# Kernel tuning notes

Measured on AMD Instinct MI355X. Metric: run time of the kernel, lower is better.

The kernel has to match this reference:

```python
import jax, jax.numpy as jnp
import numpy as np

DIM = 512
NUM_HEADS = 8
HEAD_DIM = DIM // NUM_HEADS
EPS = 1e-12  # F.normalize eps


def _l2norm(x):
    # F.normalize(x, dim=-1): x / max(||x||, eps)
    n = jnp.sqrt(jnp.sum(x * x, axis=-1, keepdims=True))
    return x / jnp.maximum(n, EPS)


def setup_inputs() -> dict:
    key = jax.random.key(0)
    ks = jax.random.split(key, 5)
    B, T, D = 4, 2048, DIM
    z = jax.random.normal(ks[0], (B, T, D), dtype=jnp.float32)
    t = jnp.zeros((1,), dtype=jnp.float32)  # unused ODE time
    omega = jax.random.normal(ks[1], (1, 1, D), dtype=jnp.float32) * 0.1
    # nn.Linear default init scale ~ U(-1/sqrt(fan_in), 1/sqrt(fan_in))
    s = 1.0 / np.sqrt(D)
    W_qk = jax.random.uniform(ks[2], (2 * D, D), jnp.float32, -s, s)
    W_out = jax.random.uniform(ks[3], (D, D), jnp.float32, -s, s)
    b_out = jax.random.uniform(ks[4], (D,), jnp.float32, -s, s)
    return {"t": t, "z": z, "omega": omega, "W_qk": W_qk, "W_out": W_out, "b_out": b_out}


def reference(t, z, omega, W_qk, W_out, b_out):
    B, T, D = z.shape
    H, hd = NUM_HEADS, HEAD_DIM
    qk = z @ W_qk.T                      # [B,T,2D]
    q, k = qk[..., :D], qk[..., D:]
    q = _l2norm(q.reshape(B, T, H, hd))  # [B,T,H,hd]
    k = _l2norm(k.reshape(B, T, H, hd))
    # coupling: [B,H,T,T]
    coupling = jnp.einsum("bqhd,bkhd->bhqk", q, k)
    interaction = jnp.sin(coupling)
    force = jnp.einsum("bhqk,bkhd->bqhd", interaction, k).reshape(B, T, D)
    return omega + force @ W_out.T + b_out
```

## Files before the change

kernel.cpp:

```cpp
#include <hip/hip_runtime.h>
#include <hip/hip_bf16.h>

typedef unsigned short u16;
typedef _Float16 f16;
typedef __attribute__((ext_vector_type(8))) _Float16 f16x8;
typedef __attribute__((ext_vector_type(2))) __fp16 h16x2;
typedef __attribute__((ext_vector_type(8))) short short8;
typedef __attribute__((ext_vector_type(4))) float f32x4;

#define B_ 4
#define T_ 2048
#define D_ 512
#define H_ 8
#define M_ (B_*T_)
#define INV2PI 0.15915494309189535f

__device__ f16 g_qb[M_*D_];
__device__ f16 g_kb[M_*D_];
__device__ f16 g_kTp[(size_t)B_*H_*64*T_];
__device__ f16 g_force[(size_t)M_*D_];

__device__ inline float sin2pi(float x) {
#if __has_builtin(__builtin_amdgcn_sinf)
  return __builtin_amdgcn_sinf(x);
#else
  return __sinf(x * 6.283185307179586f);
#endif
}

__device__ inline f16x8 cvt8h(f32x4 a, f32x4 b) {
  union { h16x2 h[4]; f16x8 v; } u;
  u.h[0] = __builtin_amdgcn_cvt_pkrtz(a[0], a[1]);
  u.h[1] = __builtin_amdgcn_cvt_pkrtz(a[2], a[3]);
  u.h[2] = __builtin_amdgcn_cvt_pkrtz(b[0], b[1]);
  u.h[3] = __builtin_amdgcn_cvt_pkrtz(b[2], b[3]);
  return u.v;
}

__device__ inline int perm5(int p) {
  int lg = p >> 3, e = p & 7;
  return (e < 4) ? lg*4 + e : 16 + lg*4 + (e & 3);
}

template<int MODE>
__global__ __launch_bounds__(256, 2)
void gemm_bt(float* __restrict__ Cout, const float* __restrict__ add1,
             const float* __restrict__ add2, const float* __restrict__ Afp,
             const float* __restrict__ Bfp) {
  constexpr int K = 512;
  constexpr int N = (MODE == 0) ? 1024 : 512;
  __shared__ f16 As[128*72];
  __shared__ f16 Bs[128*72];
  const int m0 = blockIdx.x*128, n0 = blockIdx.y*128;
  const int t = threadIdx.x;
  const int w = t>>6, l = t&63;
  const int wr = (w>>1)*64, wc = (w&1)*64;
  const int lg = l>>4, li = l&15;
  const int srow = t>>3, scol = (t&7)*8;

  f32x4 acc[4][4] = {};

  for (int k0 = 0; k0 < K; k0 += 64) {
#pragma unroll
    for (int p = 0; p < 4; ++p) {
      int r = srow + p*32;
      {
        f32x4 b0 = *(const f32x4*)&Bfp[(size_t)(n0+r)*K + k0 + scol];
        f32x4 b1 = *(const f32x4*)&Bfp[(size_t)(n0+r)*K + k0 + scol + 4];
        *(f16x8*)&Bs[r*72 + scol] = cvt8h(b0, b1);
      }
      if (MODE == 0) {
        f32x4 a0 = *(const f32x4*)&Afp[(size_t)(m0+r)*K + k0 + scol];
        f32x4 a1 = *(const f32x4*)&Afp[(size_t)(m0+r)*K + k0 + scol + 4];
        *(f16x8*)&As[r*72 + scol] = cvt8h(a0, a1);
      } else {
        *(short8*)&As[r*72 + scol] =
          *(const short8*)&g_force[(size_t)(m0+r)*K + k0 + scol];
      }
    }
    __syncthreads();
#pragma unroll
    for (int ks = 0; ks < 2; ++ks) {
      f16x8 af[4], bf[4];
#pragma unroll
      for (int i = 0; i < 4; ++i)
        af[i] = *(const f16x8*)&As[(wr + i*16 + li)*72 + ks*32 + lg*8];
#pragma unroll
      for (int j = 0; j < 4; ++j)
        bf[j] = *(const f16x8*)&Bs[(wc + j*16 + li)*72 + ks*32 + lg*8];
#pragma unroll
      for (int i = 0; i < 4; ++i)
#pragma unroll
        for (int j = 0; j < 4; ++j)
          acc[i][j] = __builtin_amdgcn_mfma_f32_16x16x32_f16(af[i], bf[j], acc[i][j], 0, 0, 0);
    }
    __syncthreads();
  }

  if (MODE == 0) {
    const bool isq = (n0 < 512);
    f16* dst = isq ? g_qb : g_kb;
    const float qs = isq ? INV2PI : 1.0f;
    const int nb = (isq ? n0 : n0 - 512) + wc;
#pragma unroll
    for (int i = 0; i < 4; ++i) {
#pragma unroll
      for (int r = 0; r < 4; ++r) {
        float s = 0.f;
#pragma unroll
        for (int j = 0; j < 4; ++j) s += acc[i][j][r]*acc[i][j][r];
#pragma unroll
        for (int off = 1; off < 16; off <<= 1) s += __shfl_xor(s, off);
        float sc = qs / fmaxf(sqrtf(s), 1e-12f);
        int row = m0 + wr + i*16 + lg*4 + r;
#pragma unroll
        for (int j = 0; j < 4; ++j)
          dst[(size_t)row*D_ + nb + j*16 + li] = (f16)(acc[i][j][r]*sc);
      }
    }
  } else {
#pragma unroll
    for (int i = 0; i < 4; ++i) {
#pragma unroll
      for (int j = 0; j < 4; ++j) {
        int col = n0 + wc + j*16 + li;
        float badd = add1[col] + add2[col];
#pragma unroll
        for (int r = 0; r < 4; ++r) {
          int row = m0 + wr + i*16 + lg*4 + r;
          Cout[(size_t)row*N + col] = acc[i][j][r] + badd;
        }
      }
    }
  }
}

__global__ void transpose_k_kernel() {
  __shared__ u16 tile[64*72];
  const int t0 = blockIdx.x*64, bh = blockIdx.y;
  const int b = bh>>3, h = bh&7;
  const int t = threadIdx.x;
  const u16* kb = (const u16*)g_kb;
  u16* kT = (u16*)g_kTp;
  {
    int r = t>>2, cs = (t&3)*16;
    const u16* src = kb + (size_t)(b*T_ + t0 + r)*D_ + h*64 + cs;
    *(short8*)&tile[r*72 + cs]     = *(const short8*)(src);
    *(short8*)&tile[r*72 + cs + 8] = *(const short8*)(src + 8);
  }
  __syncthreads();
  {
    int d = t>>2, ts = (t&3)*16;
    short8 o0, o1;
#pragma unroll
    for (int j = 0; j < 8; ++j) {
      int p0 = ts + j, p1 = ts + 8 + j;
      int s0 = (p0 & ~31) | perm5(p0 & 31);
      int s1 = (p1 & ~31) | perm5(p1 & 31);
      o0[j] = (short)tile[s0*72 + d];
      o1[j] = (short)tile[s1*72 + d];
    }
    u16* dst = kT + ((size_t)bh*64 + d)*T_ + t0 + ts;
    *(short8*)(dst)     = o0;
    *(short8*)(dst + 8) = o1;
  }
}

__global__ __launch_bounds__(256)
void kuramoto_attn_kernel() {
  __shared__ u16 Ks[2][128*72];
  __shared__ u16 KTs[2][64*136];
  const int wg  = blockIdx.x;
  const int wgp = (wg & 7)*32 + (wg >> 3);
  const int bh = wgp >> 3, qt = wgp & 7;
  const int b = bh >> 3, h = bh & 7;
  const int t = threadIdx.x;
  const int w = t>>6, l = t&63;
  const int lg = l>>4, li = l&15;

  f16x8 bq[2][4];
#pragma unroll
  for (int ks = 0; ks < 2; ++ks)
#pragma unroll
    for (int j = 0; j < 4; ++j)
      bq[ks][j] = *(const f16x8*)&g_qb[(size_t)(b*T_ + qt*256 + w*64 + j*16 + li)*D_
                                       + h*64 + ks*32 + lg*8];

  const int sr = t>>3, sc = (t&7)*8;
  const int sd = t>>4, sk = (t&15)*8;
  const u16* kbase = (const u16*)g_kb  + (size_t)b*T_*D_ + h*64;
  const u16* tbase = (const u16*)g_kTp + (size_t)bh*64*T_;

  f32x4 acc_o[4][4] = {};

#pragma unroll
  for (int p = 0; p < 4; ++p) {
    *(short8*)&Ks[0][(sr + p*32)*72 + sc] =
      *(const short8*)&kbase[(size_t)(sr + p*32)*D_ + sc];
    *(short8*)&KTs[0][(sd + p*16)*136 + sk] =
      *(const short8*)&tbase[(size_t)(sd + p*16)*T_ + sk];
  }
  __syncthreads();

#define QK_STEP(KKP, S) do {                                                   \
  _Pragma("unroll") for (int ks = 0; ks < 2; ++ks) {                           \
    f16x8 af0 = *(const f16x8*)&Ks[buf][((2*(KKP)  )*16 + li)*72 + ks*32 + lg*8]; \
    f16x8 af1 = *(const f16x8*)&Ks[buf][((2*(KKP)+1)*16 + li)*72 + ks*32 + lg*8]; \
    _Pragma("unroll") for (int j = 0; j < 4; ++j) {                            \
      S[0][j] = __builtin_amdgcn_mfma_f32_16x16x32_f16(af0, bq[ks][j], S[0][j], 0,0,0); \
      S[1][j] = __builtin_amdgcn_mfma_f32_16x16x32_f16(af1, bq[ks][j], S[1][j], 0,0,0); \
    } } } while(0)

#define SINPV_STEP(KKP, S) do {                                                \
  f16x8 apv[4];                                                                \
  _Pragma("unroll") for (int j = 0; j < 4; ++j) {                              \
    union { h16x2 h[4]; f16x8 v; } cv;                                         \
    cv.h[0] = __builtin_amdgcn_cvt_pkrtz(sin2pi(S[0][j][0]), sin2pi(S[0][j][1])); \
    cv.h[1] = __builtin_amdgcn_cvt_pkrtz(sin2pi(S[0][j][2]), sin2pi(S[0][j][3])); \
    cv.h[2] = __builtin_amdgcn_cvt_pkrtz(sin2pi(S[1][j][0]), sin2pi(S[1][j][1])); \
    cv.h[3] = __builtin_amdgcn_cvt_pkrtz(sin2pi(S[1][j][2]), sin2pi(S[1][j][3])); \
    apv[j] = cv.v; }                                                           \
  _Pragma("unroll") for (int di = 0; di < 4; ++di) {                           \
    f16x8 bv = *(const f16x8*)&KTs[buf][(di*16 + li)*136 + (KKP)*32 + lg*8];   \
    _Pragma("unroll") for (int j = 0; j < 4; ++j)                              \
      acc_o[j][di] = __builtin_amdgcn_mfma_f32_16x16x32_f16(apv[j], bv, acc_o[j][di], 0,0,0); \
  } } while(0)

#pragma unroll 2
  for (int ii = 0; ii < 16; ++ii) {
    const int buf = ii & 1;
    short8 rk[4], rt[4];
    if (ii < 15) {
      const int ktn = ii + 1;
#pragma unroll
      for (int p = 0; p < 4; ++p) {
        rk[p] = *(const short8*)&kbase[(size_t)(ktn*128 + sr + p*32)*D_ + sc];
        rt[p] = *(const short8*)&tbase[(size_t)(sd + p*16)*T_ + ktn*128 + sk];
      }
    }

    f32x4 sA[2][4] = {};
    f32x4 sB[2][4] = {};
    QK_STEP(0, sA);
    QK_STEP(1, sB);  SINPV_STEP(0, sA);
#pragma unroll
    for (int z = 0; z < 2; ++z)
#pragma unroll
      for (int j = 0; j < 4; ++j) sA[z][j] = (f32x4)(0.f);
    QK_STEP(2, sA);  SINPV_STEP(1, sB);
#pragma unroll
    for (int z = 0; z < 2; ++z)
#pragma unroll
      for (int j = 0; j < 4; ++j) sB[z][j] = (f32x4)(0.f);
    QK_STEP(3, sB);  SINPV_STEP(2, sA);
                     SINPV_STEP(3, sB);

    if (ii < 15) {
#pragma unroll
      for (int p = 0; p < 4; ++p) {
        *(short8*)&Ks[buf^1][(sr + p*32)*72 + sc] = rk[p];
        *(short8*)&KTs[buf^1][(sd + p*16)*136 + sk] = rt[p];
      }
    }
    __syncthreads();
  }
#undef QK_STEP
#undef SINPV_STEP

#pragma unroll
  for (int j = 0; j < 4; ++j)
#pragma unroll
    for (int di = 0; di < 4; ++di)
#pragma unroll
      for (int r = 0; r < 4; ++r) {
        int row = b*T_ + qt*256 + w*64 + j*16 + lg*4 + r;
        int col = h*64 + di*16 + li;
        g_force[(size_t)row*D_ + col] = (f16)acc_o[j][di][r];
      }
}

extern "C" void kernel_launch(void* const* d_in, const int* in_sizes, int n_in,
                              void* d_out, int out_size, void* d_ws, size_t ws_size,
                              hipStream_t stream) {
  const float* z     = (const float*)d_in[1];
  const float* omega = (const float*)d_in[2];
  const float* Wqk   = (const float*)d_in[3];
  const float* Wout  = (const float*)d_in[4];
  const float* bout  = (const float*)d_in[5];
  float* out = (float*)d_out;

  gemm_bt<0><<<dim3(M_/128, 1024/128), 256, 0, stream>>>(nullptr, nullptr, nullptr, z, Wqk);
  transpose_k_kernel<<<dim3(T_/64, B_*H_), 256, 0, stream>>>();
  kuramoto_attn_kernel<<<256, 256, 0, stream>>>();
  gemm_bt<1><<<dim3(M_/128, 512/128), 256, 0, stream>>>(out, omega, bout, nullptr, Wout);
}
```

Baseline: 155.3 us.

## Split attention over key halves and remap GEMM blocks across XCDs

The attention kernel now splits the key sequence into two halves, so 512 workgroups run instead of 256. Each half writes a partial force buffer, and the output GEMM adds the two when it loads its A operand. This is meant to fill the 256 CUs more evenly, which 256 workgroups did not. MFMA sections also get s_setprio hints, and the GEMM grids become 1D with an XCD-aware block mapping to improve L2 locality. The cost is an extra fp16 partial buffer, its write and read traffic, and fp16 rounding of two partial sums instead of one.

```diff
diff --git a/kernel.cpp b/kernel.cpp
--- a/kernel.cpp
+++ b/kernel.cpp
@@ -18,7 +18,8 @@
 __device__ f16 g_qb[M_*D_];
 __device__ f16 g_kb[M_*D_];
 __device__ f16 g_kTp[(size_t)B_*H_*64*T_];
-__device__ f16 g_force[(size_t)M_*D_];
+__device__ f16 g_fA[(size_t)M_*D_];
+__device__ f16 g_fB[(size_t)M_*D_];
 
 __device__ inline float sin2pi(float x) {
 #if __has_builtin(__builtin_amdgcn_sinf)
@@ -49,9 +50,14 @@
              const float* __restrict__ Bfp) {
   constexpr int K = 512;
   constexpr int N = (MODE == 0) ? 1024 : 512;
+  constexpr int NB = N/128;
   __shared__ f16 As[128*72];
   __shared__ f16 Bs[128*72];
-  const int m0 = blockIdx.x*128, n0 = blockIdx.y*128;
+  const int bidx = blockIdx.x;
+  const int xcd = bidx & 7, idx = bidx >> 3;
+  const int mp = xcd + 8*(idx/NB);
+  const int np = idx % NB;
+  const int m0 = mp*128, n0 = np*128;
   const int t = threadIdx.x;
   const int w = t>>6, l = t&63;
   const int wr = (w>>1)*64, wc = (w&1)*64;
@@ -74,8 +80,9 @@
         f32x4 a1 = *(const f32x4*)&Afp[(size_t)(m0+r)*K + k0 + scol + 4];
         *(f16x8*)&As[r*72 + scol] = cvt8h(a0, a1);
       } else {
-        *(short8*)&As[r*72 + scol] =
-          *(const short8*)&g_force[(size_t)(m0+r)*K + k0 + scol];
+        f16x8 a = *(const f16x8*)&g_fA[(size_t)(m0+r)*K + k0 + scol];
+        f16x8 c = *(const f16x8*)&g_fB[(size_t)(m0+r)*K + k0 + scol];
+        *(f16x8*)&As[r*72 + scol] = a + c;
       }
     }
     __syncthreads();
@@ -166,13 +173,13 @@
   }
 }
 
-__global__ __launch_bounds__(256)
+__global__ __launch_bounds__(256, 2)
 void kuramoto_attn_kernel() {
   __shared__ u16 Ks[2][128*72];
   __shared__ u16 KTs[2][64*136];
   const int wg  = blockIdx.x;
-  const int wgp = (wg & 7)*32 + (wg >> 3);
-  const int bh = wgp >> 3, qt = wgp & 7;
+  const int wgp = (wg & 7)*64 + (wg >> 3);
+  const int bh = wgp >> 4, qt = (wgp & 15) >> 1, kh = wgp & 1;
   const int b = bh >> 3, h = bh & 7;
   const int t = threadIdx.x;
   const int w = t>>6, l = t&63;
@@ -190,15 +197,16 @@
   const int sd = t>>4, sk = (t&15)*8;
   const u16* kbase = (const u16*)g_kb  + (size_t)b*T_*D_ + h*64;
   const u16* tbase = (const u16*)g_kTp + (size_t)bh*64*T_;
+  const int kt0 = kh*8;
 
   f32x4 acc_o[4][4] = {};
 
 #pragma unroll
   for (int p = 0; p < 4; ++p) {
     *(short8*)&Ks[0][(sr + p*32)*72 + sc] =
-      *(const short8*)&kbase[(size_t)(sr + p*32)*D_ + sc];
+      *(const short8*)&kbase[(size_t)(kt0*128 + sr + p*32)*D_ + sc];
     *(short8*)&KTs[0][(sd + p*16)*136 + sk] =
-      *(const short8*)&tbase[(size_t)(sd + p*16)*T_ + sk];
+      *(const short8*)&tbase[(size_t)(sd + p*16)*T_ + kt0*128 + sk];
   }
   __syncthreads();
 
@@ -206,10 +214,12 @@
   _Pragma("unroll") for (int ks = 0; ks < 2; ++ks) {                           \
     f16x8 af0 = *(const f16x8*)&Ks[buf][((2*(KKP)  )*16 + li)*72 + ks*32 + lg*8]; \
     f16x8 af1 = *(const f16x8*)&Ks[buf][((2*(KKP)+1)*16 + li)*72 + ks*32 + lg*8]; \
+    __builtin_amdgcn_s_setprio(1);                                             \
     _Pragma("unroll") for (int j = 0; j < 4; ++j) {                            \
       S[0][j] = __builtin_amdgcn_mfma_f32_16x16x32_f16(af0, bq[ks][j], S[0][j], 0,0,0); \
       S[1][j] = __builtin_amdgcn_mfma_f32_16x16x32_f16(af1, bq[ks][j], S[1][j], 0,0,0); \
-    } } } while(0)
+    }                                                                          \
+    __builtin_amdgcn_s_setprio(0); } } while(0)
 
 #define SINPV_STEP(KKP, S) do {                                                \
   f16x8 apv[4];                                                                \
@@ -222,16 +232,18 @@
     apv[j] = cv.v; }                                                           \
   _Pragma("unroll") for (int di = 0; di < 4; ++di) {                           \
     f16x8 bv = *(const f16x8*)&KTs[buf][(di*16 + li)*136 + (KKP)*32 + lg*8];   \
+    __builtin_amdgcn_s_setprio(1);                                             \
     _Pragma("unroll") for (int j = 0; j < 4; ++j)                              \
       acc_o[j][di] = __builtin_amdgcn_mfma_f32_16x16x32_f16(apv[j], bv, acc_o[j][di], 0,0,0); \
+    __builtin_amdgcn_s_setprio(0);                                             \
   } } while(0)
 
 #pragma unroll 2
-  for (int ii = 0; ii < 16; ++ii) {
+  for (int ii = 0; ii < 8; ++ii) {
     const int buf = ii & 1;
     short8 rk[4], rt[4];
-    if (ii < 15) {
-      const int ktn = ii + 1;
+    if (ii < 7) {
+      const int ktn = kt0 + ii + 1;
 #pragma unroll
       for (int p = 0; p < 4; ++p) {
         rk[p] = *(const short8*)&kbase[(size_t)(ktn*128 + sr + p*32)*D_ + sc];
@@ -255,7 +267,7 @@
     QK_STEP(3, sB);  SINPV_STEP(2, sA);
                      SINPV_STEP(3, sB);
 
-    if (ii < 15) {
+    if (ii < 7) {
 #pragma unroll
       for (int p = 0; p < 4; ++p) {
         *(short8*)&Ks[buf^1][(sr + p*32)*72 + sc] = rk[p];
@@ -267,6 +279,7 @@
 #undef QK_STEP
 #undef SINPV_STEP
 
+  f16* F = kh ? g_fB : g_fA;
 #pragma unroll
   for (int j = 0; j < 4; ++j)
 #pragma unroll
@@ -275,7 +288,7 @@
       for (int r = 0; r < 4; ++r) {
         int row = b*T_ + qt*256 + w*64 + j*16 + lg*4 + r;
         int col = h*64 + di*16 + li;
-        g_force[(size_t)row*D_ + col] = (f16)acc_o[j][di][r];
+        F[(size_t)row*D_ + col] = (f16)acc_o[j][di][r];
       }
 }
 
@@ -289,8 +302,8 @@
   const float* bout  = (const float*)d_in[5];
   float* out = (float*)d_out;
 
-  gemm_bt<0><<<dim3(M_/128, 1024/128), 256, 0, stream>>>(nullptr, nullptr, nullptr, z, Wqk);
+  gemm_bt<0><<<512, 256, 0, stream>>>(nullptr, nullptr, nullptr, z, Wqk);
   transpose_k_kernel<<<dim3(T_/64, B_*H_), 256, 0, stream>>>();
-  kuramoto_attn_kernel<<<256, 256, 0, stream>>>();
-  gemm_bt<1><<<dim3(M_/128, 512/128), 256, 0, stream>>>(out, omega, bout, nullptr, Wout);
-}
+  kuramoto_attn_kernel<<<512, 256, 0, stream>>>();
+  gemm_bt<1><<<256, 256, 0, stream>>>(out, omega, bout, nullptr, Wout);
+}
```

Result: slower. 163.9 us (+5.5%).
